# Performance work log

Measured on AMD Instinct MI355X. Metric: run time of the kernel, lower is better.

Reference implementation:

```python
import jax, jax.numpy as jnp
import numpy as np

B, C, L = 8, 512, 8192
H = 8  # head_count
DK = C // H  # head key channels
DV = C // H  # head value channels


def setup_inputs() -> dict:
    key = jax.random.key(0)
    ks = jax.random.split(key, 10)
    s = 1.0 / np.sqrt(C)
    return {
        "input_": jax.random.normal(ks[0], (B, C, L), jnp.float32),
        "context_": jax.random.normal(ks[1], (B, C, L), jnp.float32),
        "Wk": jax.random.normal(ks[2], (C, C), jnp.float32) * s,
        "bk": jax.random.normal(ks[3], (C,), jnp.float32) * 0.01,
        "Wq": jax.random.normal(ks[4], (C, C), jnp.float32) * s,
        "bq": jax.random.normal(ks[5], (C,), jnp.float32) * 0.01,
        "Wv": jax.random.normal(ks[6], (C, C), jnp.float32) * s,
        "bv": jax.random.normal(ks[7], (C,), jnp.float32) * 0.01,
        "Wr": jax.random.normal(ks[8], (C, C), jnp.float32) * s,
        "br": jax.random.normal(ks[9], (C,), jnp.float32) * 0.01,
    }


def _proj(W, b, x):
    # 1x1 Conv1d == channel matmul: [O,C] x [B,C,L] -> [B,O,L]
    return jnp.einsum('oc,bcl->bol', W, x) + b[None, :, None]


def reference(input_, context_, Wk, bk, Wq, bq, Wv, bv, Wr, br):
    b, _, l = input_.shape
    keys = _proj(Wk, bk, context_).reshape(b, H, DK, l)
    queries = _proj(Wq, bq, input_).reshape(b, H, DK, l)
    values = _proj(Wv, bv, context_).reshape(b, H, DV, l)
    # per-head: softmax(K) over sequence, softmax(Q) over head-key channels
    k = jax.nn.softmax(keys, axis=3)
    q = jax.nn.softmax(queries, axis=2)
    # context = K @ V^T : [b,h,dk,dv]
    ctx = jnp.einsum('bhkl,bhvl->bhkv', k, values)
    # attended = context^T @ Q : [b,h,dv,l]
    att = jnp.einsum('bhkv,bhkl->bhvl', ctx, q).reshape(b, H * DV, l)
    return _proj(Wr, br, att) + input_
```

## Files before the change

kernel.cpp:

```cpp
#include <hip/hip_runtime.h>

#define NB 8
#define NC 512
#define NL 8192
#define NH 8
#define ND 64

typedef float f32x4 __attribute__((ext_vector_type(4)));
typedef __bf16 bf16x8 __attribute__((ext_vector_type(8)));
typedef unsigned int u32x4 __attribute__((ext_vector_type(4)));

__device__ __forceinline__ unsigned short f2bf(float f) {
    unsigned u = __builtin_bit_cast(unsigned, f);
    u += 0x7fffu + ((u >> 16) & 1u);
    return (unsigned short)(u >> 16);
}
__device__ __forceinline__ bf16x8 frag_from_u32x4(u32x4 v) {
    return __builtin_bit_cast(bf16x8, v);
}
__device__ __forceinline__ bf16x8 ld_frag_lds(const unsigned short* p) {
    const unsigned* q = (const unsigned*)p;
    u32x4 v = { q[0], q[1], q[2], q[3] };
    return frag_from_u32x4(v);
}
__device__ __forceinline__ bf16x8 ld_frag_g16(const unsigned short* p) {
    return frag_from_u32x4(*(const u32x4*)p);
}

__device__ __forceinline__ void gload16(const unsigned short* g, unsigned short* l) {
    __builtin_amdgcn_global_load_lds(
        (const __attribute__((address_space(1))) unsigned int*)g,
        (__attribute__((address_space(3))) unsigned int*)l, 16, 0, 0);
}

__device__ __forceinline__ void prep_body(int i,
    const float* __restrict__ Wk, const float* __restrict__ Wv,
    const float* __restrict__ Wq, const float* __restrict__ Wr,
    const float* __restrict__ bk, const float* __restrict__ bv,
    unsigned short* __restrict__ Wb, float* __restrict__ bkv, float* __restrict__ zf)
{
    const int WN = NC * NC;
    if (i < 4 * WN) {
        const float* src = (i < WN) ? Wk : (i < 2 * WN) ? Wv : (i < 3 * WN) ? Wq : Wr;
        Wb[i] = f2bf(src[i & (WN - 1)]);
    } else if (i < 4 * WN + 2 * NC) {
        int j = i - 4 * WN;
        bkv[j] = (j < NC) ? bk[j] : bv[j - NC];
    } else {
        zf[i - (4 * WN + 2 * NC)] = 0.f;
    }
}

__device__ __forceinline__ int ltidx(int c, int l) {
    return c * 64 + ((((l) >> 2) ^ ((c >> 2) & 15)) << 2) + (l & 3);
}
__global__ __launch_bounds__(256) void transpose_prep_kernel(
    const float* __restrict__ X0, const float* __restrict__ X1,
    unsigned short* __restrict__ Y0, unsigned short* __restrict__ Y1,
    const float* __restrict__ Wk, const float* __restrict__ Wv,
    const float* __restrict__ Wq, const float* __restrict__ Wr,
    const float* __restrict__ bk, const float* __restrict__ bv,
    unsigned short* __restrict__ Wb, float* __restrict__ bkv, float* __restrict__ zf)
{
    const int bz = blockIdx.z;
    const int t = threadIdx.x;
    if (bz == 2 * NB) {
        constexpr int total = 4 * NC * NC + 2 * NC + (NB * NH * ND * ND + NB * NC);
        const int stride = (NL / 64) * (NC / 64) * 256;
        for (int i = (blockIdx.y * (NL / 64) + blockIdx.x) * 256 + t; i < total; i += stride)
            prep_body(i, Wk, Wv, Wq, Wr, bk, bv, Wb, bkv, zf);
        return;
    }
    const float* X = (bz < NB) ? X0 : X1;
    unsigned short* Y = (bz < NB) ? Y0 : Y1;
    const int b = bz & (NB - 1);
    const int l0 = blockIdx.x * 64, c0 = blockIdx.y * 64;
    __shared__ alignas(16) unsigned short lt[64 * 64];
    const float* Xb = X + (size_t)b * NC * NL;
    #pragma unroll
    for (int it = 0; it < 4; ++it) {
        const int c = it * 16 + (t >> 4), l4 = (t & 15) * 4;
        f32x4 v = *(const f32x4*)(Xb + (size_t)(c0 + c) * NL + l0 + l4);
        unsigned lo = f2bf(v.x) | ((unsigned)f2bf(v.y) << 16);
        unsigned hi = f2bf(v.z) | ((unsigned)f2bf(v.w) << 16);
        unsigned* p = (unsigned*)&lt[ltidx(c, l4)];
        p[0] = lo; p[1] = hi;
    }
    __syncthreads();
    unsigned short* Yb = Y + (size_t)b * NL * NC;
    #pragma unroll
    for (int it = 0; it < 2; ++it) {
        const int l = it * 32 + (t >> 3), c8 = (t & 7) * 8;
        u32x4 o;
        #pragma unroll
        for (int d = 0; d < 4; ++d) {
            unsigned lo = lt[ltidx(c8 + 2 * d, l)];
            unsigned hi = lt[ltidx(c8 + 2 * d + 1, l)];
            o[d] = lo | (hi << 16);
        }
        *(u32x4*)(Yb + (size_t)(l0 + l) * NC + c0 + c8) = o;
    }
}

template<int MT, bool RESID, bool PERB, bool QSMT, bool EXPK>
__global__ __launch_bounds__(256) void gemm_kernel(
    const unsigned short* __restrict__ Wb,
    const unsigned short* __restrict__ Xt,
    const float* __restrict__ bias,
    const float* __restrict__ resid,
    void* __restrict__ Yv)
{
    const int bx = blockIdx.x;
    const int g  = bx >> 3;
    const int mt = g % MT;
    const int nt = (g / MT) * 8 + (bx & 7);
    const int b  = blockIdx.y;
    const int t  = threadIdx.x;
    const int wave = t >> 6, lane = t & 63;
    const int m0 = mt * 128, n0 = nt * 128;
    const int wm = (wave & 1) * 64, wn = (wave >> 1) * 64;
    const int OC = MT * 128;

    __shared__ alignas(16) unsigned short lA[128 * 32];
    __shared__ alignas(16) unsigned short lX[128 * 32];

    f32x4 acc[4][4] = {};

    const unsigned short* Wp = Wb + (PERB ? (size_t)b * NC * NC : 0);
    const unsigned short* Xb = Xt + (size_t)b * NL * NC;

    const int lr = lane & 15, q = lane >> 4;
    const unsigned aoff = (unsigned)((wm + lr) * 64 + (q ^ (((wm + lr) >> 1) & 3)) * 16);
    const unsigned boff = (unsigned)((wn + lr) * 64 + (q ^ (((wn + lr) >> 1) & 3)) * 16);
    const int pb0 = wave * 128;

    for (int k0 = 0; k0 < NC; k0 += 32) {
        #pragma unroll
        for (int cc = 0; cc < 2; ++cc) {
            const int pb = pb0 + cc * 64;
            const int p  = pb + lane;
            const int r  = p >> 2;
            const int qq = (p & 3) ^ ((r >> 1) & 3);
            gload16(Wp + (size_t)(m0 + r) * NC + k0 + qq * 8, &lA[pb * 8]);
            gload16(Xb + (size_t)(n0 + r) * NC + k0 + qq * 8, &lX[pb * 8]);
        }
        __syncthreads();

        bf16x8 af[4], bfx[4];
        #pragma unroll
        for (int i = 0; i < 4; ++i)
            af[i] = frag_from_u32x4(*(const u32x4*)((const char*)lA + aoff + i * 1024));
        #pragma unroll
        for (int j = 0; j < 4; ++j)
            bfx[j] = frag_from_u32x4(*(const u32x4*)((const char*)lX + boff + j * 1024));
        #pragma unroll
        for (int i = 0; i < 4; ++i)
            #pragma unroll
            for (int j = 0; j < 4; ++j)
                acc[i][j] = __builtin_amdgcn_mfma_f32_16x16x32_bf16(af[i], bfx[j], acc[i][j], 0, 0, 0);
        __syncthreads();
    }

    const int col = lane & 15, row0 = (lane >> 4) * 4;

    if constexpr (QSMT) {
        #pragma unroll
        for (int i = 0; i < 4; ++i)
            #pragma unroll
            for (int r = 0; r < 4; ++r) {
                const float bo = bias[m0 + wm + i * 16 + row0 + r];
                #pragma unroll
                for (int j = 0; j < 4; ++j) acc[i][j][r] += bo;
            }
        float inv[4];
        #pragma unroll
        for (int j = 0; j < 4; ++j) {
            float m = -1e30f;
            #pragma unroll
            for (int i = 0; i < 4; ++i)
                #pragma unroll
                for (int r = 0; r < 4; ++r) m = fmaxf(m, acc[i][j][r]);
            m = fmaxf(m, __shfl_xor(m, 16));
            m = fmaxf(m, __shfl_xor(m, 32));
            float s = 0.f;
            #pragma unroll
            for (int i = 0; i < 4; ++i)
                #pragma unroll
                for (int r = 0; r < 4; ++r) {
                    const float e = __expf(acc[i][j][r] - m);
                    acc[i][j][r] = e;
                    s += e;
                }
            s += __shfl_xor(s, 16);
            s += __shfl_xor(s, 32);
            inv[j] = 1.0f / s;
        }
        unsigned short* Yq = (unsigned short*)Yv;
        #pragma unroll
        for (int j = 0; j < 4; ++j) {
            const size_t rowb = (size_t)b * NL * NC + (size_t)(n0 + wn + j * 16 + col) * NC;
            #pragma unroll
            for (int i = 0; i < 4; ++i) {
                const int o0 = m0 + wm + i * 16 + row0;
                unsigned lo = f2bf(acc[i][j][0] * inv[j]) | ((unsigned)f2bf(acc[i][j][1] * inv[j]) << 16);
                unsigned hi = f2bf(acc[i][j][2] * inv[j]) | ((unsigned)f2bf(acc[i][j][3] * inv[j]) << 16);
                *(unsigned long long*)(Yq + rowb + o0) =
                    (unsigned long long)lo | ((unsigned long long)hi << 32);
            }
        }
    } else if constexpr (EXPK) {
        unsigned short* Y = (unsigned short*)Yv;
        if (m0 < NC) {
            #pragma unroll
            for (int i = 0; i < 4; ++i)
                #pragma unroll
                for (int r = 0; r < 4; ++r) {
                    const int o = m0 + wm + i * 16 + row0 + r;
                    const float bo = bias[o];
                    const size_t rb = (size_t)b * OC * NL + (size_t)o * NL + n0 + wn;
                    #pragma unroll
                    for (int j = 0; j < 4; ++j)
                        Y[rb + j * 16 + col] = f2bf(__expf(acc[i][j][r] + bo));
                }
        } else {
            #pragma unroll
            for (int i = 0; i < 4; ++i)
                #pragma unroll
                for (int r = 0; r < 4; ++r) {
                    const int o = m0 + wm + i * 16 + row0 + r;
                    const float bo = bias[o];
                    const size_t rb = (size_t)b * OC * NL + (size_t)o * NL + n0 + wn;
                    #pragma unroll
                    for (int j = 0; j < 4; ++j)
                        Y[rb + j * 16 + col] = f2bf(acc[i][j][r] + bo);
                }
        }
    } else {
        #pragma unroll
        for (int i = 0; i < 4; ++i) {
            #pragma unroll
            for (int r = 0; r < 4; ++r) {
                const int o = m0 + wm + i * 16 + row0 + r;
                const float bo = bias[o];
                const size_t rb = (size_t)b * OC * NL + (size_t)o * NL + n0 + wn;
                if constexpr (RESID) {
                    float* Y = (float*)Yv;
                    #pragma unroll
                    for (int j = 0; j < 4; ++j) {
                        const size_t idx = rb + j * 16 + col;
                        Y[idx] = acc[i][j][r] + bo + resid[idx];
                    }
                } else {
                    unsigned short* Y = (unsigned short*)Yv;
                    #pragma unroll
                    for (int j = 0; j < 4; ++j)
                        Y[rb + j * 16 + col] = f2bf(acc[i][j][r] + bo);
                }
            }
        }
    }
}

__global__ __launch_bounds__(256) void ctx_kernel(
    const unsigned short* __restrict__ KV,
    float* __restrict__ ctx,
    float* __restrict__ rowsum)
{
    const int bh = blockIdx.x;
    const int sp = blockIdx.y;
    const int t = threadIdx.x;
    const int wave = t >> 6, lane = t & 63;
    const int b = bh >> 3, h = bh & 7;
    const size_t base_k = ((size_t)b * 2 * NC + h * ND) * NL;
    const size_t base_v = base_k + (size_t)NC * NL;
    const int i = wave * 16 + (lane & 15);
    const int koff = (lane >> 4) * 8;
    const unsigned short* Ka = KV + base_k + (size_t)i * NL + koff;

    const u32x4 onesw = { 0x3f803f80u, 0x3f803f80u, 0x3f803f80u, 0x3f803f80u };
    const bf16x8 onef = frag_from_u32x4(onesw);

    f32x4 acc[4] = {};
    f32x4 accs = {};
    const int l0 = sp * (NL / 16);
    for (int l = l0; l < l0 + (NL / 16); l += 32) {
        bf16x8 a = ld_frag_g16(Ka + l);
        #pragma unroll
        for (int j = 0; j < 4; ++j) {
            bf16x8 bv = ld_frag_g16(KV + base_v + (size_t)(j * 16 + (lane & 15)) * NL + l + koff);
            acc[j] = __builtin_amdgcn_mfma_f32_16x16x32_bf16(a, bv, acc[j], 0, 0, 0);
        }
        accs = __builtin_amdgcn_mfma_f32_16x16x32_bf16(a, onef, accs, 0, 0, 0);
    }
    const int col = lane & 15, row0 = (lane >> 4) * 4;
    #pragma unroll
    for (int j = 0; j < 4; ++j)
        #pragma unroll
        for (int r = 0; r < 4; ++r)
            atomicAdd(&ctx[(size_t)bh * (ND * ND) + (size_t)(wave * 16 + row0 + r) * ND + j * 16 + col],
                      acc[j][r]);
    if (col == 0) {
        #pragma unroll
        for (int r = 0; r < 4; ++r)
            atomicAdd(&rowsum[(size_t)b * NC + h * ND + wave * 16 + row0 + r], accs[r]);
    }
}

__global__ __launch_bounds__(512) void fold_kernel(
    const unsigned short* __restrict__ Wrb,
    const float* __restrict__ ctxb,
    const float* __restrict__ rowsum,
    unsigned short* __restrict__ Mb)
{
    const int bh = blockIdx.x;
    const int b = bh >> 3, h = bh & 7;
    const int t = threadIdx.x;
    const int wave = t >> 6, lane = t & 63;

    __shared__ unsigned short lc[64 * 66];
    const float* cs = ctxb + (size_t)bh * (ND * ND);
    const float* rs = rowsum + (size_t)b * NC + h * ND;
    #pragma unroll
    for (int it = 0; it < 8; ++it) {
        int i = it * 512 + t;
        lc[(i >> 6) * 66 + (i & 63)] = f2bf(cs[i] / rs[i >> 6]);
    }
    __syncthreads();

    const int koff = (lane >> 4) * 8;
    f32x4 acc[4][4] = {};
    #pragma unroll
    for (int kk = 0; kk < 64; kk += 32) {
        bf16x8 af[4], bfx[4];
        #pragma unroll
        for (int i = 0; i < 4; ++i)
            af[i] = ld_frag_g16(Wrb + (size_t)(wave * 64 + i * 16 + (lane & 15)) * NC
                                + h * ND + kk + koff);
        #pragma unroll
        for (int j = 0; j < 4; ++j)
            bfx[j] = ld_frag_lds(&lc[(j * 16 + (lane & 15)) * 66 + kk + koff]);
        #pragma unroll
        for (int i = 0; i < 4; ++i)
            #pragma unroll
            for (int j = 0; j < 4; ++j)
                acc[i][j] = __builtin_amdgcn_mfma_f32_16x16x32_bf16(af[i], bfx[j], acc[i][j], 0, 0, 0);
    }

    const int col = lane & 15, row0 = (lane >> 4) * 4;
    #pragma unroll
    for (int i = 0; i < 4; ++i)
        #pragma unroll
        for (int r = 0; r < 4; ++r) {
            const int o = wave * 64 + i * 16 + row0 + r;
            #pragma unroll
            for (int j = 0; j < 4; ++j)
                Mb[(size_t)b * NC * NC + (size_t)o * NC + h * ND + j * 16 + col]
                    = f2bf(acc[i][j][r]);
        }
}

extern "C" void kernel_launch(void* const* d_in, const int* in_sizes, int n_in,
                              void* d_out, int out_size, void* d_ws, size_t ws_size,
                              hipStream_t stream) {
    (void)in_sizes; (void)n_in; (void)out_size; (void)ws_size;
    const float* input_   = (const float*)d_in[0];
    const float* context_ = (const float*)d_in[1];
    const float* Wk = (const float*)d_in[2];
    const float* bk = (const float*)d_in[3];
    const float* Wq = (const float*)d_in[4];
    const float* bq = (const float*)d_in[5];
    const float* Wv = (const float*)d_in[6];
    const float* bv = (const float*)d_in[7];
    const float* Wr = (const float*)d_in[8];
    const float* br = (const float*)d_in[9];
    float* out = (float*)d_out;

    char* ws = (char*)d_ws;
    unsigned short* Wkvb = (unsigned short*)ws;
    unsigned short* Wqb  = Wkvb + 2 * NC * NC;
    unsigned short* Wrb  = Wqb + NC * NC;
    float* bkv  = (float*)(Wrb + NC * NC);
    float* ctxb = bkv + 2 * NC;
    float* rowsum = ctxb + NB * NH * ND * ND;
    unsigned short* KVp = (unsigned short*)(rowsum + NB * NC);
    unsigned short* R2  = KVp + (size_t)NB * 2 * NC * NL;
    unsigned short* Mb  = KVp;
    unsigned short* Xt_in = (unsigned short*)d_out;

    transpose_prep_kernel<<<dim3(NL / 64, NC / 64, 2 * NB + 1), 256, 0, stream>>>(
        context_, input_, R2, Xt_in,
        Wk, Wv, Wq, Wr, bk, bv, Wkvb, bkv, ctxb);

    gemm_kernel<8, false, false, false, true><<<dim3(64 * 8, NB), 256, 0, stream>>>(
        Wkvb, R2, bkv, nullptr, KVp);

    gemm_kernel<4, false, false, true, false><<<dim3(64 * 4, NB), 256, 0, stream>>>(
        Wqb, Xt_in, bq, nullptr, R2);

    ctx_kernel<<<dim3(NB * NH, 16), 256, 0, stream>>>(KVp, ctxb, rowsum);
    fold_kernel<<<NB * NH, 512, 0, stream>>>(Wrb, ctxb, rowsum, Mb);

    gemm_kernel<4, true, true, false, false><<<dim3(64 * 4, NB), 256, 0, stream>>>(
        Mb, R2, br, input_, out);
}
```

Baseline: 675.1 us.

## Add 256x256-tile 8-wave GEMM with double-buffered LDS for KV and output projections

Adds a new GEMM kernel with 512 threads, 256x256 output tiles and 128 KB of double-buffered LDS. It streams operands with direct global-to-LDS loads using an XOR swizzle, and interleaves staging with MFMA phases under explicit barriers and wave priority. The KV projection and the final output projection now use this kernel, raising arithmetic intensity per block and cutting operand reloads. The cost is a single block per CU because of the large LDS footprint, fewer blocks overall (1024 and 512), and more register pressure from 128 accumulator floats per thread.

```diff
diff --git a/kernel.cpp b/kernel.cpp
--- a/kernel.cpp
+++ b/kernel.cpp
@@ -25,6 +25,9 @@
 }
 __device__ __forceinline__ bf16x8 ld_frag_g16(const unsigned short* p) {
     return frag_from_u32x4(*(const u32x4*)p);
+}
+__device__ __forceinline__ bf16x8 ldL(const unsigned short* Lb, unsigned off) {
+    return frag_from_u32x4(*(const u32x4*)((const char*)Lb + off));
 }
 
 __device__ __forceinline__ void gload16(const unsigned short* g, unsigned short* l) {
@@ -99,6 +102,165 @@
             o[d] = lo | (hi << 16);
         }
         *(u32x4*)(Yb + (size_t)(l0 + l) * NC + c0 + c8) = o;
+    }
+}
+
+__device__ __forceinline__ void stage_half(
+    unsigned short* __restrict__ Ld, const unsigned short* __restrict__ Gs,
+    int t, int wave)
+{
+    #pragma unroll
+    for (int c = 0; c < 2; ++c) {
+        const int idx = c * 512 + t;
+        const int r = idx >> 3;
+        const int ch = (idx & 7) ^ (r & 7);
+        gload16(Gs + (size_t)r * NC + ch * 8, Ld + (size_t)(c * 512 + wave * 64) * 8);
+    }
+}
+
+template<int MT, bool RESID, bool PERB, bool EXPK>
+__global__ __launch_bounds__(512) void gemm8_kernel(
+    const unsigned short* __restrict__ Wb,
+    const unsigned short* __restrict__ Xt,
+    const float* __restrict__ bias,
+    const float* __restrict__ resid,
+    void* __restrict__ Yv)
+{
+    const int bx = blockIdx.x;
+    const int g  = bx >> 3;
+    const int mt = g % MT;
+    const int nt = (g / MT) * 8 + (bx & 7);
+    const int b  = blockIdx.y;
+    const int t  = threadIdx.x;
+    const int wave = t >> 6, lane = t & 63;
+    const int m0 = mt * 256, n0 = nt * 256;
+    const int wm = wave >> 2, wn = wave & 3;
+    const int OC = MT * 256;
+
+    __shared__ alignas(16) unsigned short L[65536];
+
+    f32x4 acc[8][4] = {};
+
+    const unsigned short* Wp = Wb + (PERB ? (size_t)b * NC * NC : 0) + (size_t)m0 * NC;
+    const unsigned short* Xp = Xt + (size_t)b * NL * NC + (size_t)n0 * NC;
+
+    const int lr = lane & 15, qg = lane >> 4;
+    const unsigned xr = (unsigned)(lr & 7);
+    const unsigned cq0 = (((unsigned)qg) ^ xr) * 16u;
+    const unsigned cq1 = (((unsigned)qg + 4u) ^ xr) * 16u;
+    const unsigned aB = (unsigned)(wm * 16384 + lr * 128);
+    const unsigned bB = 32768u + (unsigned)((wn >> 1) * 16384 + ((wn & 1) * 64 + lr) * 128);
+
+    #define STA(par, half, kt) stage_half(&L[(par) * 32768 + (half) * 8192], \
+        Wp + (size_t)((half) * 128) * NC + (kt) * 64, t, wave)
+    #define STB(par, half, kt) stage_half(&L[(par) * 32768 + 16384 + (half) * 8192], \
+        Xp + (size_t)((half) * 128) * NC + (kt) * 64, t, wave)
+
+    STA(0, 0, 0); STA(0, 1, 0); STB(0, 0, 0); STB(0, 1, 0);
+    STA(1, 0, 1); STA(1, 1, 1); STB(1, 0, 1); STB(1, 1, 1);
+    __builtin_amdgcn_sched_barrier(0);
+    asm volatile("s_waitcnt vmcnt(8)" ::: "memory");
+    __builtin_amdgcn_sched_barrier(0);
+    __builtin_amdgcn_s_barrier();
+    __builtin_amdgcn_sched_barrier(0);
+
+    for (int kt = 0; kt < 8; ++kt) {
+        const unsigned parB = (unsigned)((kt & 1) * 65536);
+        const int par = kt & 1, ks = kt + 2;
+        bf16x8 bf[4][2];
+        #pragma unroll
+        for (int q4 = 0; q4 < 4; ++q4) {
+            if (q4 == 0) {
+                #pragma unroll
+                for (int j = 0; j < 4; ++j) {
+                    bf[j][0] = ldL(L, parB + bB + j * 2048 + cq0);
+                    bf[j][1] = ldL(L, parB + bB + j * 2048 + cq1);
+                }
+            }
+            bf16x8 af[2][2];
+            #pragma unroll
+            for (int di = 0; di < 2; ++di) {
+                af[di][0] = ldL(L, parB + aB + (q4 * 2 + di) * 2048 + cq0);
+                af[di][1] = ldL(L, parB + aB + (q4 * 2 + di) * 2048 + cq1);
+            }
+            if (ks < 8) {
+                if (q4 == 1)      { STB(par, 0, ks); }
+                else if (q4 == 2) { STB(par, 1, ks); }
+                else if (q4 == 3) { STA(par, 0, ks); STA(par, 1, ks); }
+            }
+            __builtin_amdgcn_sched_barrier(0);
+            __builtin_amdgcn_s_barrier();
+            __builtin_amdgcn_sched_barrier(0);
+            __builtin_amdgcn_s_setprio(1);
+            #pragma unroll
+            for (int di = 0; di < 2; ++di)
+                #pragma unroll
+                for (int j = 0; j < 4; ++j) {
+                    acc[q4 * 2 + di][j] = __builtin_amdgcn_mfma_f32_16x16x32_bf16(
+                        af[di][0], bf[j][0], acc[q4 * 2 + di][j], 0, 0, 0);
+                    acc[q4 * 2 + di][j] = __builtin_amdgcn_mfma_f32_16x16x32_bf16(
+                        af[di][1], bf[j][1], acc[q4 * 2 + di][j], 0, 0, 0);
+                }
+            __builtin_amdgcn_s_setprio(0);
+            __builtin_amdgcn_sched_barrier(0);
+            if (q4 == 3) {
+                if (kt < 6)       asm volatile("s_waitcnt vmcnt(8)" ::: "memory");
+                else if (kt == 6) asm volatile("s_waitcnt vmcnt(0)" ::: "memory");
+                __builtin_amdgcn_sched_barrier(0);
+            }
+            __builtin_amdgcn_s_barrier();
+            __builtin_amdgcn_sched_barrier(0);
+        }
+    }
+    #undef STA
+    #undef STB
+
+    const int col = lr, row0 = qg * 4;
+    if constexpr (EXPK) {
+        unsigned short* Y = (unsigned short*)Yv;
+        const bool isK = (m0 < NC);
+        #pragma unroll
+        for (int i = 0; i < 8; ++i)
+            #pragma unroll
+            for (int r = 0; r < 4; ++r) {
+                const int o = m0 + wm * 128 + i * 16 + row0 + r;
+                const float bo = bias[o];
+                const size_t rb = (size_t)b * OC * NL + (size_t)o * NL + n0 + wn * 64;
+                #pragma unroll
+                for (int j = 0; j < 4; ++j) {
+                    float v = acc[i][j][r] + bo;
+                    if (isK) v = __expf(v);
+                    Y[rb + j * 16 + col] = f2bf(v);
+                }
+            }
+    } else if constexpr (RESID) {
+        float* Y = (float*)Yv;
+        #pragma unroll
+        for (int i = 0; i < 8; ++i)
+            #pragma unroll
+            for (int r = 0; r < 4; ++r) {
+                const int o = m0 + wm * 128 + i * 16 + row0 + r;
+                const float bo = bias[o];
+                const size_t rb = (size_t)b * OC * NL + (size_t)o * NL + n0 + wn * 64;
+                #pragma unroll
+                for (int j = 0; j < 4; ++j) {
+                    const size_t idx = rb + j * 16 + col;
+                    Y[idx] = acc[i][j][r] + bo + resid[idx];
+                }
+            }
+    } else {
+        unsigned short* Y = (unsigned short*)Yv;
+        #pragma unroll
+        for (int i = 0; i < 8; ++i)
+            #pragma unroll
+            for (int r = 0; r < 4; ++r) {
+                const int o = m0 + wm * 128 + i * 16 + row0 + r;
+                const float bo = bias[o];
+                const size_t rb = (size_t)b * OC * NL + (size_t)o * NL + n0 + wn * 64;
+                #pragma unroll
+                for (int j = 0; j < 4; ++j)
+                    Y[rb + j * 16 + col] = f2bf(acc[i][j][r] + bo);
+            }
     }
 }
 
@@ -210,31 +372,21 @@
         }
     } else if constexpr (EXPK) {
         unsigned short* Y = (unsigned short*)Yv;
-        if (m0 < NC) {
-            #pragma unroll
-            for (int i = 0; i < 4; ++i)
-                #pragma unroll
-                for (int r = 0; r < 4; ++r) {
-                    const int o = m0 + wm + i * 16 + row0 + r;
-                    const float bo = bias[o];
-                    const size_t rb = (size_t)b * OC * NL + (size_t)o * NL + n0 + wn;
-                    #pragma unroll
-                    for (int j = 0; j < 4; ++j)
-                        Y[rb + j * 16 + col] = f2bf(__expf(acc[i][j][r] + bo));
-                }
-        } else {
-            #pragma unroll
-            for (int i = 0; i < 4; ++i)
-                #pragma unroll
-                for (int r = 0; r < 4; ++r) {
-                    const int o = m0 + wm + i * 16 + row0 + r;
-                    const float bo = bias[o];
-                    const size_t rb = (size_t)b * OC * NL + (size_t)o * NL + n0 + wn;
-                    #pragma unroll
-                    for (int j = 0; j < 4; ++j)
-                        Y[rb + j * 16 + col] = f2bf(acc[i][j][r] + bo);
-                }
-        }
+        const bool isK = (m0 < NC);
+        #pragma unroll
+        for (int i = 0; i < 4; ++i)
+            #pragma unroll
+            for (int r = 0; r < 4; ++r) {
+                const int o = m0 + wm + i * 16 + row0 + r;
+                const float bo = bias[o];
+                const size_t rb = (size_t)b * OC * NL + (size_t)o * NL + n0 + wn;
+                #pragma unroll
+                for (int j = 0; j < 4; ++j) {
+                    float v = acc[i][j][r] + bo;
+                    if (isK) v = __expf(v);
+                    Y[rb + j * 16 + col] = f2bf(v);
+                }
+            }
     } else {
         #pragma unroll
         for (int i = 0; i < 4; ++i) {
@@ -391,15 +543,15 @@
         context_, input_, R2, Xt_in,
         Wk, Wv, Wq, Wr, bk, bv, Wkvb, bkv, ctxb);
 
-    gemm_kernel<8, false, false, false, true><<<dim3(64 * 8, NB), 256, 0, stream>>>(
+    gemm8_kernel<4, false, false, true><<<dim3(128, NB), 512, 0, stream>>>(
         Wkvb, R2, bkv, nullptr, KVp);
 
-    gemm_kernel<4, false, false, true, false><<<dim3(64 * 4, NB), 256, 0, stream>>>(
+    gemm_kernel<4, false, false, true, false><<<dim3(256, NB), 256, 0, stream>>>(
         Wqb, Xt_in, bq, nullptr, R2);
 
     ctx_kernel<<<dim3(NB * NH, 16), 256, 0, stream>>>(KVp, ctxb, rowsum);
     fold_kernel<<<NB * NH, 512, 0, stream>>>(Wrb, ctxb, rowsum, Mb);
 
-    gemm_kernel<4, true, true, false, false><<<dim3(64 * 4, NB), 256, 0, stream>>>(
+    gemm8_kernel<2, true, true, false><<<dim3(64, NB), 512, 0, stream>>>(
         Mb, R2, br, input_, out);
 }
```

After: 621.8 us. 1.09x faster.
